# Kernel optimization log

Measured on AMD Instinct MI355X. Metric: run time of the kernel, lower is better.

Reference implementation:

```python
import jax, jax.numpy as jnp
import numpy as np

B, KVH, HPK, D = 4, 8, 4, 128          # batch, n_kv_heads, n_heads_per_kv, head_size
SEQ_KV = 4096                           # cached history length
SEQ = SEQ_KV + 1                        # history + current token
K, LOCAL_K, SINK, RANK = 512, 128, 4, 32


def gather(t, axis, i):
    """Broadcasting take_along_axis, mirroring the torch `gather` helper."""
    axis = axis % t.ndim
    tgt = list(t.shape)
    tgt[axis] = i.shape[axis]
    return jnp.take_along_axis(t, jnp.broadcast_to(i, tgt), axis)


def sparse_q_score(q, key_cpu_t, cur_key_t):
    # q: (B,KVH,HPK,1,D); key_cpu_t: (B,KVH,D,SEQ_KV); cur_key_t: (B,KVH,1,D,1)
    absq = jnp.abs(q).sum(2, keepdims=True)                    # (B,KVH,1,1,D)
    _, idx = jax.lax.top_k(absq, RANK)                         # (B,KVH,1,1,RANK)
    q_proj = gather(q, -1, idx)                                # (B,KVH,HPK,1,RANK)
    idx_t = jnp.swapaxes(idx, -1, -2)                          # (B,KVH,1,RANK,1)
    k_hist = gather(key_cpu_t[:, :, None], -2, idx_t)          # (B,KVH,1,RANK,SEQ_KV)
    k_cur = gather(cur_key_t, -2, idx_t)                       # (B,KVH,1,RANK,1)
    k_proj = jnp.concatenate([k_hist, k_cur], -1)              # (B,KVH,1,RANK,SEQ)
    scale = jnp.sqrt(jnp.abs(q_proj).sum(-1) / jnp.abs(q).sum(-1) * D)[..., None]
    return jnp.matmul(q_proj, k_proj) / scale                  # (B,KVH,HPK,1,SEQ)


def setup_inputs():
    key = jax.random.key(0)
    ks = jax.random.split(key, 6)
    query = jax.random.normal(ks[0], (B, KVH * HPK, 1, D), jnp.float32)
    k = jax.random.normal(ks[1], (B, KVH, 1, D), jnp.float32)
    v = jax.random.normal(ks[2], (B, KVH, 1, D), jnp.float32)
    logmask = jnp.zeros((B, KVH * HPK, 1, SEQ), jnp.float32)
    key_cpu = jax.random.normal(ks[3], (B, KVH, SEQ_KV, D), jnp.float32)
    value_cpu = jax.random.normal(ks[4], (B, KVH, SEQ_KV, D), jnp.float32)
    s_key_cpu = jnp.swapaxes(key_cpu, -1, -2)                  # head-size-contiguous copy
    mean_v = jax.random.normal(ks[5], (B, KVH, 1, 1, D), jnp.float32)
    return {"query": query, "key": k, "value": v, "logmask": logmask,
            "key_cpu": key_cpu, "value_cpu": value_cpu,
            "s_key_cpu": s_key_cpu, "mean_v": mean_v}


def reference(query, key, value, logmask, key_cpu, value_cpu, s_key_cpu, mean_v):
    q = query.reshape(B, KVH, HPK, 1, D)
    k = key.reshape(B, KVH, 1, 1, D)
    v = value.reshape(B, KVH, 1, 1, D)
    lm = logmask.reshape(B, KVH, HPK, 1, SEQ)
    # approximate scores over the full key history + current key
    score = (sparse_q_score(q, s_key_cpu, jnp.swapaxes(k, 3, 4)) + lm).astype(jnp.float32)
    # causal index over history (excluding current token): 0 = most recent unmasked
    neg = jnp.isneginf(lm[..., :-1])
    ci = jnp.where(neg, -1,
                   jnp.cumsum((~neg)[..., ::-1].astype(jnp.int32), -1)[..., ::-1] - 1)
    is_local = (0 <= ci) & (ci < LOCAL_K)
    is_sink = ci >= SEQ - SINK - 1
    fmax = jnp.finfo(jnp.float32).max
    topk_score = jnp.where(is_local | is_sink, fmax, score[..., :-1]).sum(2, keepdims=True)
    kk = min(K + SINK, SEQ)
    _, indices = jax.lax.top_k(topk_score, kk)                 # (B,KVH,1,1,kk)
    # running mean value update
    mean_v_new = (mean_v * (SEQ - 1) + v.astype(jnp.float32)) / SEQ
    # weight reallocation to the mean value
    norm = jax.nn.softmax(score, -1)
    kv_weight = gather(norm, -1, indices).sum(-1) + norm[..., -1]  # (B,KVH,HPK,1)
    # gather selected K/V and append current token
    kv_idx = indices[..., 0, :, None]                          # (B,KVH,1,kk,1)
    key_g = jnp.concatenate([gather(key_cpu[:, :, None], -2, kv_idx), k], -2)   # (B,KVH,1,kk+1,D)
    val_g = jnp.concatenate([gather(value_cpu[:, :, None], -2, kv_idx), v], -2)
    cur_idx = jnp.full(indices.shape[:-1] + (1,), SEQ - 1, indices.dtype)
    lm_g = gather(lm, -1, jnp.concatenate([indices, cur_idx], -1))  # (B,KVH,HPK,1,kk+1)
    # dense attention over the reduced key set
    scores = jnp.matmul(q, jnp.swapaxes(key_g, -1, -2)) * (D ** -0.5) + lm_g
    weights = jax.nn.softmax(scores.astype(jnp.float32), -1) * kv_weight[..., None]
    out = jnp.matmul(weights, val_g) + (1.0 - kv_weight[..., None]) * mean_v_new
    return out.reshape(B, KVH * HPK, 1, D), weights.reshape(B, KVH * HPK, 1, kk + 1)
```

## Files before the change

### kernel.cpp

```cpp
#include <hip/hip_runtime.h>
#include <hip/hip_bf16.h>
#include <math.h>

#define NBH 32
#define HPKN 4
#define DN 128
#define SEQKV 4096
#define SEQN 4097
#define SSTR 4100
#define RANKN 32
#define KSEL 516
#define SINKN 4
#define LOCALK 128
#define NMASK 132
#define NTOP 384

__global__ __launch_bounds__(128) void k1_prep(
    const float* __restrict__ q, const float* __restrict__ key,
    const float* __restrict__ lm,
    float* __restrict__ qp_scaled, int* __restrict__ sidx_g,
    float* __restrict__ scores) {
  int bh = blockIdx.x;
  int b = bh >> 3, h = bh & 7;
  int d = threadIdx.x;
  __shared__ float qv[4][128];
  __shared__ float absq[128];
  __shared__ int sel[RANKN];
  __shared__ float red[128];
  __shared__ float scale_s[4];

  float a = 0.f;
  for (int p = 0; p < 4; ++p) {
    float val = q[((b * 32 + h * 4 + p) << 7) + d];
    qv[p][d] = val;
    a += fabsf(val);
  }
  absq[d] = a;
  __syncthreads();

  int rank = 0;
  for (int e = 0; e < 128; ++e) {
    float ae = absq[e];
    rank += (ae > a) || (ae == a && e < d);
  }
  if (rank < RANKN) sel[rank] = d;
  __syncthreads();

  for (int p = 0; p < 4; ++p) {
    red[d] = fabsf(qv[p][d]);
    __syncthreads();
    for (int s = 64; s > 0; s >>= 1) { if (d < s) red[d] += red[d + s]; __syncthreads(); }
    float full = red[0];
    __syncthreads();
    red[d] = (d < RANKN) ? fabsf(qv[p][sel[d]]) : 0.f;
    __syncthreads();
    for (int s = 64; s > 0; s >>= 1) { if (d < s) red[d] += red[d + s]; __syncthreads(); }
    if (d == 0) scale_s[p] = sqrtf(red[0] / full * 128.f);
    __syncthreads();
    if (d < RANKN) qp_scaled[(bh * 4 + p) * RANKN + d] = qv[p][sel[d]] / scale_s[p];
    __syncthreads();
  }
  if (d < RANKN) sidx_g[bh * RANKN + d] = sel[d];

  float keyv = (d < RANKN) ? key[bh * 128 + sel[d]] : 0.f;
  for (int p = 0; p < 4; ++p) {
    red[d] = (d < RANKN) ? (qv[p][sel[d]] / scale_s[p]) * keyv : 0.f;
    __syncthreads();
    for (int s = 64; s > 0; s >>= 1) { if (d < s) red[d] += red[d + s]; __syncthreads(); }
    if (d == 0)
      scores[(size_t)(bh * 4 + p) * SSTR + SEQKV] =
          red[0] + lm[(size_t)(b * 32 + h * 4 + p) * SEQN + SEQKV];
    __syncthreads();
  }
}

__global__ __launch_bounds__(256) void k2_scores(
    const float* __restrict__ skey, const float* __restrict__ lm,
    const float* __restrict__ qp_scaled, const int* __restrict__ sidx_g,
    float* __restrict__ scores, float* __restrict__ tk) {
  int bh = blockIdx.y;
  int b = bh >> 3, h = bh & 7;
  int s0 = blockIdx.x << 9;
  int t = threadIdx.x;
  __shared__ float qp[4][RANKN];
  __shared__ int sel[RANKN];
  if (t < 128) qp[t >> 5][t & 31] = qp_scaled[bh * 128 + t];
  if (t < RANKN) sel[t] = sidx_g[bh * RANKN + t];
  __syncthreads();
  const float* kb = skey + (size_t)bh * 128 * 4096;
  float a00 = 0, a01 = 0, a02 = 0, a03 = 0;
  float a10 = 0, a11 = 0, a12 = 0, a13 = 0;
#pragma unroll 4
  for (int r = 0; r < RANKN; ++r) {
    const float* row = kb + ((size_t)sel[r] << 12) + s0;
    float k0 = row[t];
    float k1 = row[t + 256];
    float q0 = qp[0][r], q1 = qp[1][r], q2 = qp[2][r], q3 = qp[3][r];
    a00 += q0 * k0; a01 += q1 * k0; a02 += q2 * k0; a03 += q3 * k0;
    a10 += q0 * k1; a11 += q1 * k1; a12 += q2 * k1; a13 += q3 * k1;
  }
  float acc0[4] = {a00, a01, a02, a03};
  float acc1[4] = {a10, a11, a12, a13};
  {
    int s = s0 + t;
    float sum = 0;
    for (int p = 0; p < 4; ++p) {
      float sc = acc0[p] + lm[(size_t)(b * 32 + h * 4 + p) * SEQN + s];
      scores[(size_t)(bh * 4 + p) * SSTR + s] = sc;
      sum += sc;
    }
    tk[(bh << 12) + s] = sum;
  }
  {
    int s = s0 + t + 256;
    float sum = 0;
    for (int p = 0; p < 4; ++p) {
      float sc = acc1[p] + lm[(size_t)(b * 32 + h * 4 + p) * SEQN + s];
      scores[(size_t)(bh * 4 + p) * SSTR + s] = sc;
      sum += sc;
    }
    tk[(bh << 12) + s] = sum;
  }
}

__global__ __launch_bounds__(256) void k3_topk(
    const float* __restrict__ tk, int* __restrict__ indices) {
  int bh = blockIdx.x;
  int t = threadIdx.x;
  __shared__ unsigned us[4096];
  __shared__ unsigned hist[2048];
  __shared__ unsigned long long binlist[2048];
  __shared__ unsigned long long selk[512];
  __shared__ unsigned chunkSum[32];
  __shared__ int c1, c2, binB_s, nAbove_s, needed_s;

  for (int s = t; s < 4096; s += 256) {
    unsigned b = __float_as_uint(tk[(bh << 12) + s]);
    us[s] = (b & 0x80000000u) ? ~b : (b | 0x80000000u);
  }
  for (int i = t; i < 2048; i += 256) hist[i] = 0;
  if (t == 0) { c1 = 0; c2 = 0; }
  __syncthreads();

  for (int s = SINKN + t; s < SEQKV - LOCALK; s += 256)
    atomicAdd(&hist[us[s] >> 21], 1u);
  __syncthreads();

  if (t < 32) {
    unsigned sum = 0;
    for (int i = 0; i < 64; ++i) sum += hist[t * 64 + i];
    chunkSum[t] = sum;
  }
  __syncthreads();

  if (t < 64) {
    int lane = t;
    unsigned x = (lane < 32) ? chunkSum[lane] : 0;
    unsigned sfx = x;
    for (int off = 1; off < 64; off <<= 1) {
      unsigned y = __shfl_down(sfx, off);
      if (lane + off < 64) sfx += y;
    }
    unsigned above = sfx - x;
    bool hit = (lane < 32) && (above < NTOP) && (above + x >= NTOP);
    unsigned long long mask = __ballot(hit);
    int C = __ffsll(mask) - 1;
    unsigned aboveC = __shfl(above, C);
    unsigned h = hist[C * 64 + lane];
    unsigned sfx2 = h;
    for (int off = 1; off < 64; off <<= 1) {
      unsigned y = __shfl_down(sfx2, off);
      if (lane + off < 64) sfx2 += y;
    }
    unsigned above2 = aboveC + (sfx2 - h);
    bool hit2 = (above2 < NTOP) && (above2 + h >= NTOP);
    unsigned long long mask2 = __ballot(hit2);
    int lB = __ffsll(mask2) - 1;
    if (lane == lB) {
      binB_s = C * 64 + lane;
      nAbove_s = (int)above2;
      needed_s = NTOP - (int)above2;
    }
  }
  __syncthreads();
  unsigned B = (unsigned)binB_s;
  int nAbove = nAbove_s, needed = needed_s;

  for (int s = SINKN + t; s < SEQKV - LOCALK; s += 256) {
    unsigned u = us[s];
    unsigned bin = u >> 21;
    unsigned long long key = ((unsigned long long)u << 32) | (unsigned)(~s);
    if (bin > B) {
      selk[atomicAdd(&c1, 1)] = key;
    } else if (bin == B) {
      int pos = atomicAdd(&c2, 1);
      if (pos < 2048) binlist[pos] = key;
    }
  }
  __syncthreads();
  int m2 = c2;
  int p2 = 1;
  while (p2 < m2) p2 <<= 1;
  for (int i = m2 + t; i < p2; i += 256) binlist[i] = 0ULL;
  __syncthreads();
  for (int k = 2; k <= p2; k <<= 1)
    for (int j = k >> 1; j > 0; j >>= 1) {
      for (int i = t; i < p2; i += 256) {
        int ixj = i ^ j;
        if (ixj > i) {
          bool desc = ((i & k) == 0);
          unsigned long long a = binlist[i], bb = binlist[ixj];
          if ((a < bb) == desc) { binlist[i] = bb; binlist[ixj] = a; }
        }
      }
      __syncthreads();
    }
  for (int i = t; i < needed; i += 256) selk[nAbove + i] = binlist[i];
  for (int i = NTOP + t; i < 512; i += 256) selk[i] = 0ULL;
  __syncthreads();
  for (int k = 2; k <= 512; k <<= 1)
    for (int j = k >> 1; j > 0; j >>= 1) {
      for (int i = t; i < 512; i += 256) {
        int ixj = i ^ j;
        if (ixj > i) {
          bool desc = ((i & k) == 0);
          unsigned long long a = selk[i], bb = selk[ixj];
          if ((a < bb) == desc) { selk[i] = bb; selk[ixj] = a; }
        }
      }
      __syncthreads();
    }
  if (t < SINKN) indices[bh * KSEL + t] = t;
  for (int i = t; i < LOCALK; i += 256)
    indices[bh * KSEL + SINKN + i] = (SEQKV - LOCALK) + i;
  for (int i = t; i < NTOP; i += 256)
    indices[bh * KSEL + NMASK + i] = (int)(~(unsigned)(selk[i] & 0xFFFFFFFFu));
}

__global__ __launch_bounds__(256) void k5_qk(
    const float* __restrict__ q, const float* __restrict__ key,
    const float* __restrict__ lm, const float* __restrict__ key_cpu,
    const int* __restrict__ indices, float* __restrict__ s2_g) {
  int bh = blockIdx.y;
  int t = threadIdx.x;
  int wave = t >> 6, lane = t & 63;
  __shared__ float qs[512];
  __shared__ int sidx[KSEL];
  qs[t] = q[((size_t)bh * 4 << 7) + t];
  qs[t + 256] = q[((size_t)bh * 4 << 7) + t + 256];
  for (int j = t; j < KSEL; j += 256) sidx[j] = indices[bh * KSEL + j];
  __syncthreads();

  const float rsqd = 0.08838834764831845f;
  float q0a = qs[lane * 2], q0b = qs[lane * 2 + 1];
  float q1a = qs[128 + lane * 2], q1b = qs[128 + lane * 2 + 1];
  float q2a = qs[256 + lane * 2], q2b = qs[256 + lane * 2 + 1];
  float q3a = qs[384 + lane * 2], q3b = qs[384 + lane * 2 + 1];

  for (int i = 0; i < 10; ++i) {
    int j = (blockIdx.x << 2) + wave + 52 * i;
    if (j > KSEL) continue;
    int sj = (j < KSEL) ? sidx[j] : SEQKV;
    const float* krow = (j < KSEL)
        ? key_cpu + ((((size_t)bh << 12) + sj) << 7)
        : key + ((size_t)bh << 7);
    float2 kk = ((const float2*)krow)[lane];
    float p0 = q0a * kk.x + q0b * kk.y;
    float p1 = q1a * kk.x + q1b * kk.y;
    float p2 = q2a * kk.x + q2b * kk.y;
    float p3 = q3a * kk.x + q3b * kk.y;
    for (int off = 32; off > 0; off >>= 1) {
      p0 += __shfl_down(p0, off);
      p1 += __shfl_down(p1, off);
      p2 += __shfl_down(p2, off);
      p3 += __shfl_down(p3, off);
    }
    if (lane == 0) {
      size_t lmb = (size_t)bh * 4 * SEQN + sj;
      s2_g[(bh * 4 + 0) * 520 + j] = p0 * rsqd + lm[lmb + 0 * SEQN];
      s2_g[(bh * 4 + 1) * 520 + j] = p1 * rsqd + lm[lmb + 1 * SEQN];
      s2_g[(bh * 4 + 2) * 520 + j] = p2 * rsqd + lm[lmb + 2 * SEQN];
      s2_g[(bh * 4 + 3) * 520 + j] = p3 * rsqd + lm[lmb + 3 * SEQN];
    }
  }
}

__global__ __launch_bounds__(256) void k6_stats(
    const float* __restrict__ scores, const int* __restrict__ indices,
    const float* __restrict__ s2_g, const float* __restrict__ value,
    const float* __restrict__ mean_v,
    float* __restrict__ out_w, float* __restrict__ w_g,
    float* __restrict__ out) {
  int bhp = blockIdx.x;
  int bh = bhp >> 2;
  int t = threadIdx.x;
  __shared__ int sidx[KSEL];
  __shared__ float red[256];
  __shared__ float bc;

  for (int j = t; j < KSEL; j += 256) sidx[j] = indices[bh * KSEL + j];
  __syncthreads();

  const float* srow = scores + (size_t)bhp * SSTR;
  const float4* srow4 = (const float4*)srow;
  float mx = -INFINITY;
  for (int i = t; i < 1024; i += 256) {
    float4 v = srow4[i];
    mx = fmaxf(mx, fmaxf(fmaxf(v.x, v.y), fmaxf(v.z, v.w)));
  }
  if (t == 0) mx = fmaxf(mx, srow[SEQKV]);
  red[t] = mx; __syncthreads();
  for (int st = 128; st > 0; st >>= 1) {
    if (t < st) red[t] = fmaxf(red[t], red[t + st]);
    __syncthreads();
  }
  float m = red[0]; __syncthreads();
  float se = 0.f;
  for (int i = t; i < 1024; i += 256) {
    float4 v = srow4[i];
    se += expf(v.x - m) + expf(v.y - m) + expf(v.z - m) + expf(v.w - m);
  }
  if (t == 0) se += expf(srow[SEQKV] - m);
  red[t] = se; __syncthreads();
  for (int st = 128; st > 0; st >>= 1) {
    if (t < st) red[t] += red[t + st];
    __syncthreads();
  }
  float sumexp = red[0]; __syncthreads();
  float ss = 0.f;
  for (int j = t; j < KSEL; j += 256) ss += expf(srow[sidx[j]] - m);
  red[t] = ss; __syncthreads();
  for (int st = 128; st > 0; st >>= 1) {
    if (t < st) red[t] += red[t + st];
    __syncthreads();
  }
  float kvw;
  if (t == 0) bc = (red[0] + expf(srow[SEQKV] - m)) / sumexp;
  __syncthreads();
  kvw = bc; __syncthreads();

  const float* s2r = s2_g + (size_t)bhp * 520;
  float mx2 = -INFINITY;
  for (int j = t; j < KSEL + 1; j += 256) mx2 = fmaxf(mx2, s2r[j]);
  red[t] = mx2; __syncthreads();
  for (int st = 128; st > 0; st >>= 1) {
    if (t < st) red[t] = fmaxf(red[t], red[t + st]);
    __syncthreads();
  }
  float m2 = red[0]; __syncthreads();
  float se2 = 0.f;
  for (int j = t; j < KSEL + 1; j += 256) se2 += expf(s2r[j] - m2);
  red[t] = se2; __syncthreads();
  for (int st = 128; st > 0; st >>= 1) {
    if (t < st) red[t] += red[t + st];
    __syncthreads();
  }
  float inv = kvw / red[0];

  for (int j = t; j < KSEL + 1; j += 256) {
    float w = expf(s2r[j] - m2) * inv;
    out_w[(size_t)bhp * (KSEL + 1) + j] = w;
    w_g[(size_t)bhp * 520 + j] = w;
  }

  if (t < 128) {
    float vcur = value[((size_t)bh << 7) + t];
    float mvn = (mean_v[((size_t)bh << 7) + t] * 4096.f + vcur) / 4097.f;
    out[((size_t)bhp << 7) + t] = (1.f - kvw) * mvn;
  }
}

__global__ __launch_bounds__(256) void k7_wv(
    const float* __restrict__ value, const float* __restrict__ value_cpu,
    const int* __restrict__ indices, const float* __restrict__ w_g,
    float* __restrict__ out) {
  int bh = blockIdx.y;
  int c0 = blockIdx.x << 6;
  int t = threadIdx.x;
  int d = t & 127, half = t >> 7;
  __shared__ int sidx[64];
  __shared__ float wsh[4][64];
  __shared__ float red[2][4][128];

  int nj = min(64, KSEL + 1 - c0);
  if (t < nj) {
    int j = c0 + t;
    sidx[t] = (j < KSEL) ? indices[bh * KSEL + j] : -1;
  }
  for (int i = t; i < 4 * 64; i += 256) {
    int p = i >> 6, jl = i & 63;
    wsh[p][jl] = (jl < nj) ? w_g[(size_t)(bh * 4 + p) * 520 + c0 + jl] : 0.f;
  }
  __syncthreads();

  float a0 = 0, a1 = 0, a2 = 0, a3 = 0;
  for (int jl = half; jl < nj; jl += 2) {
    int sj = sidx[jl];
    const float* vrow = (sj >= 0)
        ? value_cpu + ((((size_t)bh << 12) + sj) << 7)
        : value + ((size_t)bh << 7);
    float v = vrow[d];
    a0 += wsh[0][jl] * v;
    a1 += wsh[1][jl] * v;
    a2 += wsh[2][jl] * v;
    a3 += wsh[3][jl] * v;
  }
  red[half][0][d] = a0; red[half][1][d] = a1;
  red[half][2][d] = a2; red[half][3][d] = a3;
  __syncthreads();
  if (half == 0) {
#pragma unroll
    for (int p = 0; p < 4; ++p) {
      float s = red[0][p][d] + red[1][p][d];
      atomicAdd(&out[(size_t)(bh * 4 + p) * 128 + d], s);
    }
  }
}

extern "C" void kernel_launch(void* const* d_in, const int* in_sizes, int n_in,
                              void* d_out, int out_size, void* d_ws, size_t ws_size,
                              hipStream_t stream) {
  const float* query     = (const float*)d_in[0];
  const float* key       = (const float*)d_in[1];
  const float* value     = (const float*)d_in[2];
  const float* logmask   = (const float*)d_in[3];
  const float* key_cpu   = (const float*)d_in[4];
  const float* value_cpu = (const float*)d_in[5];
  const float* s_key_cpu = (const float*)d_in[6];
  const float* mean_v    = (const float*)d_in[7];

  float* out   = (float*)d_out;
  float* out_w = out + 16384;

  char* ws = (char*)d_ws;
  float* qp_scaled = (float*)ws;
  int*   sidx      = (int*)(ws + 16384);
  int*   indices   = (int*)(ws + 20480);
  float* scores    = (float*)(ws + 86528);
  float* tk        = (float*)(ws + 2185728);
  float* s2_g      = (float*)(ws + 2710016);
  float* w_g       = (float*)(ws + 2976256);

  hipLaunchKernelGGL(k1_prep, dim3(NBH), dim3(128), 0, stream,
                     query, key, logmask, qp_scaled, sidx, scores);
  hipLaunchKernelGGL(k2_scores, dim3(8, NBH), dim3(256), 0, stream,
                     s_key_cpu, logmask, qp_scaled, sidx, scores, tk);
  hipLaunchKernelGGL(k3_topk, dim3(NBH), dim3(256), 0, stream,
                     tk, indices);
  hipLaunchKernelGGL(k5_qk, dim3(13, NBH), dim3(256), 0, stream,
                     query, key, logmask, key_cpu, indices, s2_g);
  hipLaunchKernelGGL(k6_stats, dim3(128), dim3(256), 0, stream,
                     scores, indices, s2_g, value, mean_v, out_w, w_g, out);
  hipLaunchKernelGGL(k7_wv, dim3(9, NBH), dim3(256), 0, stream,
                     value, value_cpu, indices, w_g, out);
}
```

Baseline: 256.6 us.

## Fuse query prep into score kernel and use wave-aggregated atomics in top-k

Removes the separate prep kernel. Each score block now recomputes the per-head channel selection and scaled query projection itself, using wave shuffles instead of shared-memory tree reductions, and block 0 writes the current-token score. This drops one launch and the global round-trip for the projected query, at the cost of redundant prep work in all 8 blocks per head. The top-k candidate compaction also switches from per-thread shared atomics to per-wave ballot plus popcount, with one atomic per wave.

```diff
diff --git a/kernel.cpp b/kernel.cpp
--- a/kernel.cpp
+++ b/kernel.cpp
@@ -15,78 +15,61 @@
 #define NMASK 132
 #define NTOP 384
 
-__global__ __launch_bounds__(128) void k1_prep(
+__global__ __launch_bounds__(256) void k2_scores(
     const float* __restrict__ q, const float* __restrict__ key,
-    const float* __restrict__ lm,
-    float* __restrict__ qp_scaled, int* __restrict__ sidx_g,
-    float* __restrict__ scores) {
-  int bh = blockIdx.x;
-  int b = bh >> 3, h = bh & 7;
-  int d = threadIdx.x;
+    const float* __restrict__ skey, const float* __restrict__ lm,
+    float* __restrict__ scores, float* __restrict__ tk) {
+  int bh = blockIdx.y;
+  int s0 = blockIdx.x << 9;
+  int t = threadIdx.x;
+  int wave = t >> 6, lane = t & 63;
   __shared__ float qv[4][128];
   __shared__ float absq[128];
   __shared__ int sel[RANKN];
-  __shared__ float red[128];
-  __shared__ float scale_s[4];
-
-  float a = 0.f;
-  for (int p = 0; p < 4; ++p) {
-    float val = q[((b * 32 + h * 4 + p) << 7) + d];
-    qv[p][d] = val;
-    a += fabsf(val);
-  }
-  absq[d] = a;
-  __syncthreads();
-
-  int rank = 0;
-  for (int e = 0; e < 128; ++e) {
-    float ae = absq[e];
-    rank += (ae > a) || (ae == a && e < d);
-  }
-  if (rank < RANKN) sel[rank] = d;
-  __syncthreads();
-
-  for (int p = 0; p < 4; ++p) {
-    red[d] = fabsf(qv[p][d]);
-    __syncthreads();
-    for (int s = 64; s > 0; s >>= 1) { if (d < s) red[d] += red[d + s]; __syncthreads(); }
-    float full = red[0];
-    __syncthreads();
-    red[d] = (d < RANKN) ? fabsf(qv[p][sel[d]]) : 0.f;
-    __syncthreads();
-    for (int s = 64; s > 0; s >>= 1) { if (d < s) red[d] += red[d + s]; __syncthreads(); }
-    if (d == 0) scale_s[p] = sqrtf(red[0] / full * 128.f);
-    __syncthreads();
-    if (d < RANKN) qp_scaled[(bh * 4 + p) * RANKN + d] = qv[p][sel[d]] / scale_s[p];
-    __syncthreads();
-  }
-  if (d < RANKN) sidx_g[bh * RANKN + d] = sel[d];
-
-  float keyv = (d < RANKN) ? key[bh * 128 + sel[d]] : 0.f;
-  for (int p = 0; p < 4; ++p) {
-    red[d] = (d < RANKN) ? (qv[p][sel[d]] / scale_s[p]) * keyv : 0.f;
-    __syncthreads();
-    for (int s = 64; s > 0; s >>= 1) { if (d < s) red[d] += red[d + s]; __syncthreads(); }
-    if (d == 0)
-      scores[(size_t)(bh * 4 + p) * SSTR + SEQKV] =
-          red[0] + lm[(size_t)(b * 32 + h * 4 + p) * SEQN + SEQKV];
-    __syncthreads();
-  }
-}
-
-__global__ __launch_bounds__(256) void k2_scores(
-    const float* __restrict__ skey, const float* __restrict__ lm,
-    const float* __restrict__ qp_scaled, const int* __restrict__ sidx_g,
-    float* __restrict__ scores, float* __restrict__ tk) {
-  int bh = blockIdx.y;
-  int b = bh >> 3, h = bh & 7;
-  int s0 = blockIdx.x << 9;
-  int t = threadIdx.x;
   __shared__ float qp[4][RANKN];
-  __shared__ int sel[RANKN];
-  if (t < 128) qp[t >> 5][t & 31] = qp_scaled[bh * 128 + t];
-  if (t < RANKN) sel[t] = sidx_g[bh * RANKN + t];
-  __syncthreads();
+
+  {
+    float v0 = q[(size_t)bh * 512 + t];
+    float v1 = q[(size_t)bh * 512 + 256 + t];
+    qv[t >> 7][t & 127] = v0;
+    qv[2 + (t >> 7)][t & 127] = v1;
+  }
+  __syncthreads();
+  if (t < 128)
+    absq[t] = fabsf(qv[0][t]) + fabsf(qv[1][t]) + fabsf(qv[2][t]) + fabsf(qv[3][t]);
+  __syncthreads();
+  if (t < 128) {
+    float a = absq[t];
+    int rank = 0;
+    for (int e = 0; e < 128; ++e) {
+      float ae = absq[e];
+      rank += (ae > a) || (ae == a && e < t);
+    }
+    if (rank < RANKN) sel[rank] = t;
+  }
+  __syncthreads();
+  {
+    float fa = fabsf(qv[wave][lane]) + fabsf(qv[wave][lane + 64]);
+    for (int off = 32; off > 0; off >>= 1) fa += __shfl_down(fa, off);
+    float full = __shfl(fa, 0);
+    float qsel = (lane < RANKN) ? qv[wave][sel[lane]] : 0.f;
+    float sv = fabsf(qsel);
+    for (int off = 32; off > 0; off >>= 1) sv += __shfl_down(sv, off);
+    float selsum = __shfl(sv, 0);
+    float scale = sqrtf(selsum / full * 128.f);
+    if (lane < RANKN) qp[wave][lane] = qsel / scale;
+  }
+  __syncthreads();
+
+  if (blockIdx.x == 0) {
+    float kv = (lane < RANKN) ? key[bh * 128 + sel[lane]] : 0.f;
+    float pr = (lane < RANKN) ? qp[wave][lane] * kv : 0.f;
+    for (int off = 32; off > 0; off >>= 1) pr += __shfl_down(pr, off);
+    if (lane == 0)
+      scores[(size_t)(bh * 4 + wave) * SSTR + SEQKV] =
+          pr + lm[(size_t)(bh * 4 + wave) * SEQN + SEQKV];
+  }
+
   const float* kb = skey + (size_t)bh * 128 * 4096;
   float a00 = 0, a01 = 0, a02 = 0, a03 = 0;
   float a10 = 0, a11 = 0, a12 = 0, a13 = 0;
@@ -105,7 +88,7 @@
     int s = s0 + t;
     float sum = 0;
     for (int p = 0; p < 4; ++p) {
-      float sc = acc0[p] + lm[(size_t)(b * 32 + h * 4 + p) * SEQN + s];
+      float sc = acc0[p] + lm[(size_t)(bh * 4 + p) * SEQN + s];
       scores[(size_t)(bh * 4 + p) * SSTR + s] = sc;
       sum += sc;
     }
@@ -115,7 +98,7 @@
     int s = s0 + t + 256;
     float sum = 0;
     for (int p = 0; p < 4; ++p) {
-      float sc = acc1[p] + lm[(size_t)(b * 32 + h * 4 + p) * SEQN + s];
+      float sc = acc1[p] + lm[(size_t)(bh * 4 + p) * SEQN + s];
       scores[(size_t)(bh * 4 + p) * SSTR + s] = sc;
       sum += sc;
     }
@@ -127,6 +110,7 @@
     const float* __restrict__ tk, int* __restrict__ indices) {
   int bh = blockIdx.x;
   int t = threadIdx.x;
+  int lane = t & 63;
   __shared__ unsigned us[4096];
   __shared__ unsigned hist[2048];
   __shared__ unsigned long long binlist[2048];
@@ -154,30 +138,30 @@
   __syncthreads();
 
   if (t < 64) {
-    int lane = t;
-    unsigned x = (lane < 32) ? chunkSum[lane] : 0;
+    int l = t;
+    unsigned x = (l < 32) ? chunkSum[l] : 0;
     unsigned sfx = x;
     for (int off = 1; off < 64; off <<= 1) {
       unsigned y = __shfl_down(sfx, off);
-      if (lane + off < 64) sfx += y;
+      if (l + off < 64) sfx += y;
     }
     unsigned above = sfx - x;
-    bool hit = (lane < 32) && (above < NTOP) && (above + x >= NTOP);
+    bool hit = (l < 32) && (above < NTOP) && (above + x >= NTOP);
     unsigned long long mask = __ballot(hit);
     int C = __ffsll(mask) - 1;
     unsigned aboveC = __shfl(above, C);
-    unsigned h = hist[C * 64 + lane];
+    unsigned h = hist[C * 64 + l];
     unsigned sfx2 = h;
     for (int off = 1; off < 64; off <<= 1) {
       unsigned y = __shfl_down(sfx2, off);
-      if (lane + off < 64) sfx2 += y;
+      if (l + off < 64) sfx2 += y;
     }
     unsigned above2 = aboveC + (sfx2 - h);
     bool hit2 = (above2 < NTOP) && (above2 + h >= NTOP);
     unsigned long long mask2 = __ballot(hit2);
     int lB = __ffsll(mask2) - 1;
-    if (lane == lB) {
-      binB_s = C * 64 + lane;
+    if (l == lB) {
+      binB_s = C * 64 + l;
       nAbove_s = (int)above2;
       needed_s = NTOP - (int)above2;
     }
@@ -186,14 +170,27 @@
   unsigned B = (unsigned)binB_s;
   int nAbove = nAbove_s, needed = needed_s;
 
-  for (int s = SINKN + t; s < SEQKV - LOCALK; s += 256) {
-    unsigned u = us[s];
+  for (int s0 = SINKN; s0 < SEQKV - LOCALK; s0 += 256) {
+    int s = s0 + t;
+    bool valid = (s < SEQKV - LOCALK);
+    unsigned u = valid ? us[s] : 0u;
     unsigned bin = u >> 21;
+    bool win = valid && (bin > B);
+    bool bnd = valid && (bin == B);
+    unsigned long long mw = __ballot(win);
+    unsigned long long mb = __ballot(bnd);
+    int bw = 0, bb = 0;
+    if (lane == 0) {
+      if (mw) bw = atomicAdd(&c1, __popcll(mw));
+      if (mb) bb = atomicAdd(&c2, __popcll(mb));
+    }
+    bw = __shfl(bw, 0);
+    bb = __shfl(bb, 0);
+    unsigned long long lmask = (1ULL << lane) - 1ULL;
     unsigned long long key = ((unsigned long long)u << 32) | (unsigned)(~s);
-    if (bin > B) {
-      selk[atomicAdd(&c1, 1)] = key;
-    } else if (bin == B) {
-      int pos = atomicAdd(&c2, 1);
+    if (win) selk[bw + __popcll(mw & lmask)] = key;
+    if (bnd) {
+      int pos = bb + __popcll(mb & lmask);
       if (pos < 2048) binlist[pos] = key;
     }
   }
@@ -209,8 +206,8 @@
         int ixj = i ^ j;
         if (ixj > i) {
           bool desc = ((i & k) == 0);
-          unsigned long long a = binlist[i], bb = binlist[ixj];
-          if ((a < bb) == desc) { binlist[i] = bb; binlist[ixj] = a; }
+          unsigned long long a = binlist[i], bb2 = binlist[ixj];
+          if ((a < bb2) == desc) { binlist[i] = bb2; binlist[ixj] = a; }
         }
       }
       __syncthreads();
@@ -224,8 +221,8 @@
         int ixj = i ^ j;
         if (ixj > i) {
           bool desc = ((i & k) == 0);
-          unsigned long long a = selk[i], bb = selk[ixj];
-          if ((a < bb) == desc) { selk[i] = bb; selk[ixj] = a; }
+          unsigned long long a = selk[i], bb2 = selk[ixj];
+          if ((a < bb2) == desc) { selk[i] = bb2; selk[ixj] = a; }
         }
       }
       __syncthreads();
@@ -433,18 +430,14 @@
   float* out_w = out + 16384;
 
   char* ws = (char*)d_ws;
-  float* qp_scaled = (float*)ws;
-  int*   sidx      = (int*)(ws + 16384);
   int*   indices   = (int*)(ws + 20480);
   float* scores    = (float*)(ws + 86528);
   float* tk        = (float*)(ws + 2185728);
   float* s2_g      = (float*)(ws + 2710016);
   float* w_g       = (float*)(ws + 2976256);
 
-  hipLaunchKernelGGL(k1_prep, dim3(NBH), dim3(128), 0, stream,
-                     query, key, logmask, qp_scaled, sidx, scores);
   hipLaunchKernelGGL(k2_scores, dim3(8, NBH), dim3(256), 0, stream,
-                     s_key_cpu, logmask, qp_scaled, sidx, scores, tk);
+                     query, key, s_key_cpu, logmask, scores, tk);
   hipLaunchKernelGGL(k3_topk, dim3(NBH), dim3(256), 0, stream,
                      tk, indices);
   hipLaunchKernelGGL(k5_qk, dim3(13, NBH), dim3(256), 0, stream,
```

Result: faster. 248.5 us (-3.1%).
